# Performance work log

Measured on AMD Instinct MI355X. Metric: run time of the kernel, lower is better.

## Reference

```python
import jax, jax.numpy as jnp
import numpy as np

B, S, H, E = 8, 4096, 1024, 8
TEMPERATURE = 1.0


def setup_inputs() -> dict:
    key = jax.random.key(0)
    ks = jax.random.split(key, 7)
    s_h = 1.0 / np.sqrt(H).astype(np.float32)
    s_h2 = 1.0 / np.sqrt(H // 2).astype(np.float32)
    return {
        "hidden_states": jax.random.normal(ks[0], (B, S, H), jnp.float32),
        # routing_network: Linear(H, H//2) -> ReLU -> Linear(H//2, E)
        "W1": jax.random.normal(ks[1], (H, H // 2), jnp.float32) * s_h,
        "b1": jnp.zeros((H // 2,), jnp.float32),
        "W2": jax.random.normal(ks[2], (H // 2, E), jnp.float32) * s_h2,
        "b2": jnp.zeros((E,), jnp.float32),
        # per-expert dense transform (fixed stand-in for torch.randn-per-call)
        "expert_W": jax.random.normal(ks[3], (E, H, H), jnp.float32) * s_h,
        "expert_b": jax.random.normal(ks[4], (E, H), jnp.float32),
    }


def reference(hidden_states, W1, b1, W2, b2, expert_W, expert_b):
    # Routing network -> logits [B, S, E]
    h = jax.nn.relu(jnp.einsum("bsh,hf->bsf", hidden_states, W1) + b1)
    logits = jnp.einsum("bsf,fe->bse", h, W2) + b2
    probs = jax.nn.softmax(logits / TEMPERATURE, axis=-1)
    # top-1 expert per token (scores are NOT applied to output in the original)
    sel = jnp.argmax(probs, axis=-1)  # [B, S] int
    out = jnp.zeros_like(hidden_states)
    for e in range(E):  # small fixed loop over experts
        mask = (sel == e)[..., None].astype(hidden_states.dtype)  # [B, S, 1]
        xe = hidden_states * mask
        ye = jnp.einsum("bsh,hd->bsd", xe, expert_W[e]) + expert_b[e]
        out = out + ye * mask
    return out
```

## Files before the change

### kernel.cpp

```cpp
#include <hip/hip_runtime.h>
#include <hip/hip_bf16.h>
#include <stdint.h>

#define NTOK 32768
#define HD 1024
#define FD 512
#define NEXP 8
#define TAU 0.05f

typedef __attribute__((ext_vector_type(8))) short short8;
typedef __attribute__((ext_vector_type(4))) float f32x4;

__device__ __forceinline__ short f2bh(float f) {
  uint32_t u = __float_as_uint(f);
  return (short)((u + 0x7fffu + ((u >> 16) & 1u)) >> 16);
}

__device__ __forceinline__ void gl16(void* lds, const void* g) {
  __builtin_amdgcn_global_load_lds(
      (const __attribute__((address_space(1))) void*)g,
      (__attribute__((address_space(3))) void*)lds, 16, 0, 0);
}

__global__ __launch_bounds__(256) void k_convert(const float* __restrict__ x,
                                                 short* __restrict__ xbf) {
  size_t i = ((size_t)blockIdx.x * 256 + threadIdx.x) * 8;
  f32x4 v0 = *(const f32x4*)(x + i);
  f32x4 v1 = *(const f32x4*)(x + i + 4);
  short8 o;
#pragma unroll
  for (int q = 0; q < 4; ++q) { o[q] = f2bh(v0[q]); o[4 + q] = f2bh(v1[q]); }
  *(short8*)(xbf + i) = o;
}

__global__ __launch_bounds__(256) void k_transpose(
    const float* __restrict__ src, short* __restrict__ dst, int rows, int cols) {
  __shared__ float tile[32][33];
  size_t msz = (size_t)rows * cols;
  src += (size_t)blockIdx.z * msz;
  dst += (size_t)blockIdx.z * msz;
  int c0 = blockIdx.x * 32, r0 = blockIdx.y * 32;
  int tx = threadIdx.x & 31, ty = threadIdx.x >> 5;
#pragma unroll
  for (int i = 0; i < 32; i += 8)
    tile[ty + i][tx] = src[(size_t)(r0 + ty + i) * cols + c0 + tx];
  __syncthreads();
#pragma unroll
  for (int i = 0; i < 32; i += 8)
    dst[(size_t)(c0 + ty + i) * rows + r0 + tx] = f2bh(tile[tx][ty + i]);
}

template <bool ABF>
__global__ __launch_bounds__(256) void k_gemm1(
    const short* __restrict__ xbf, const float* __restrict__ xf,
    const short* __restrict__ W1T, const float* __restrict__ b1,
    const float* __restrict__ W2, float* __restrict__ part) {
  __shared__ __align__(16) char smem[37888];
  short* As = (short*)smem;
  short* Bs = (short*)(smem + 8192);

  const int tid = threadIdx.x;
  const int lane = tid & 63, wave = tid >> 6;
  const int wr = wave >> 1, wc = wave & 1;
  const int fr = lane & 15, fg = lane >> 4;
  const int bx = ((blockIdx.x & 7) << 5) | (blockIdx.x >> 3);
  const int m0 = bx * 128, n0 = blockIdx.y * 128;
  const int by = blockIdx.y;

  const int off0 = wave * 1024 + lane * 16;
  const int off1 = off0 + 4096;
  const int r0 = off0 >> 6, c0 = (off0 & 63) >> 1;
  const int r1 = off1 >> 6, c1 = (off1 & 63) >> 1;
  const short* b0p = W1T + (size_t)(n0 + r0) * HD + c0;
  const short* b1p = W1T + (size_t)(n0 + r1) * HD + c1;
  char* ldsB0 = smem + 8192 + wave * 1024;
  char* ldsB1 = smem + 8192 + wave * 1024 + 4096;

  const short* a0p = nullptr; const short* a1p = nullptr;
  char* ldsA0 = smem + wave * 1024;
  char* ldsA1 = smem + wave * 1024 + 4096;
  const float* aF = nullptr;
  int ar = 0, ah = 0;
  if constexpr (ABF) {
    a0p = xbf + (size_t)(m0 + r0) * HD + c0;
    a1p = xbf + (size_t)(m0 + r1) * HD + c1;
  } else {
    ar = tid >> 1; ah = tid & 1;
    aF = xf + (size_t)(m0 + ar) * HD + ah * 16;
  }

  f32x4 acc[4][4];
#pragma unroll
  for (int i = 0; i < 4; ++i)
#pragma unroll
    for (int j = 0; j < 4; ++j) acc[i][j] = (f32x4){0.f, 0.f, 0.f, 0.f};

  for (int k0 = 0; k0 < HD; k0 += 32) {
    gl16(ldsB0, b0p + k0);
    gl16(ldsB1, b1p + k0);
    if constexpr (ABF) {
      gl16(ldsA0, a0p + k0);
      gl16(ldsA1, a1p + k0);
    } else {
      f32x4 u0 = *(const f32x4*)(aF + k0);
      f32x4 u1 = *(const f32x4*)(aF + k0 + 4);
      f32x4 u2 = *(const f32x4*)(aF + k0 + 8);
      f32x4 u3 = *(const f32x4*)(aF + k0 + 12);
      short8 s0, s1;
#pragma unroll
      for (int q = 0; q < 4; ++q) {
        s0[q] = f2bh(u0[q]); s0[4 + q] = f2bh(u1[q]);
        s1[q] = f2bh(u2[q]); s1[4 + q] = f2bh(u3[q]);
      }
      *(short8*)(As + ar * 32 + ah * 16) = s0;
      *(short8*)(As + ar * 32 + ah * 16 + 8) = s1;
    }
    __syncthreads();
    short8 af[4], bf[4];
#pragma unroll
    for (int i = 0; i < 4; ++i) {
      af[i] = *(const short8*)(As + (wr * 64 + i * 16 + fr) * 32 + fg * 8);
      bf[i] = *(const short8*)(Bs + (wc * 64 + i * 16 + fr) * 32 + fg * 8);
    }
#pragma unroll
    for (int i = 0; i < 4; ++i)
#pragma unroll
      for (int j = 0; j < 4; ++j)
        acc[i][j] = __builtin_amdgcn_mfma_f32_16x16x32_bf16(af[i], bf[j], acc[i][j], 0, 0, 0);
    __syncthreads();
  }

  float* hl64 = (float*)smem;
  float* W2c  = (float*)(smem + 33024);
  *(f32x4*)(W2c + tid * 4) = *(const f32x4*)(W2 + (size_t)n0 * NEXP + tid * 4);
  float b1j[4];
#pragma unroll
  for (int j = 0; j < 4; ++j) b1j[j] = b1[n0 + wc * 64 + j * 16 + fr];

  for (int p = 0; p < 2; ++p) {
    if (wr == p) {
#pragma unroll
      for (int i = 0; i < 4; ++i)
#pragma unroll
        for (int j = 0; j < 4; ++j) {
          int col = wc * 64 + j * 16 + fr;
#pragma unroll
          for (int q = 0; q < 4; ++q)
            hl64[(i * 16 + fg * 4 + q) * 129 + col] = fmaxf(acc[i][j][q] + b1j[j], 0.f);
        }
    }
    __syncthreads();
    if (tid < 128) {
      int r2 = tid & 63, eh = tid >> 6;
      const float* hrow = hl64 + r2 * 129;
      const float* wcp = W2c + eh * 4;
      float s0 = 0.f, s1 = 0.f, s2 = 0.f, s3 = 0.f;
      for (int f = 0; f < 128; ++f) {
        float hv = hrow[f];
        s0 += hv * wcp[f * 8 + 0];
        s1 += hv * wcp[f * 8 + 1];
        s2 += hv * wcp[f * 8 + 2];
        s3 += hv * wcp[f * 8 + 3];
      }
      float* pp = part + (size_t)(m0 + p * 64 + r2) * 32 + by * 8 + eh * 4;
      pp[0] = s0; pp[1] = s1; pp[2] = s2; pp[3] = s3;
    }
    __syncthreads();
  }
}

__global__ __launch_bounds__(256) void k_combine(
    const float* __restrict__ part, const float* __restrict__ b2,
    int* __restrict__ sel, int* __restrict__ flagged, int* __restrict__ nflag) {
  int t = blockIdx.x * 256 + threadIdx.x;
  const float* p = part + (size_t)t * 32;
  float lg[8];
#pragma unroll
  for (int e = 0; e < 8; ++e) lg[e] = p[e] + p[8 + e] + p[16 + e] + p[24 + e] + b2[e];
  int be = 0; float best = lg[0];
#pragma unroll
  for (int e = 1; e < 8; ++e) if (lg[e] > best) { best = lg[e]; be = e; }
  float second = -3.4e38f;
#pragma unroll
  for (int e = 0; e < 8; ++e) if (e != be && lg[e] > second) second = lg[e];
  sel[t] = be;
  if (best - second < TAU) {
    int ix = atomicAdd(nflag, 1);
    if (ix < NTOK) flagged[ix] = t;
  }
}

__global__ __launch_bounds__(256) void k_recompute(
    const float* __restrict__ x, const float* __restrict__ W1,
    const float* __restrict__ b1, const float* __restrict__ W2,
    const float* __restrict__ b2, const int* __restrict__ flagged,
    const int* __restrict__ nflag, int* __restrict__ sel) {
  __shared__ float xs[1024][8];
  __shared__ double hs[8][512];
  __shared__ double lgs[8][8];
  int nf = *nflag; if (nf > NTOK) nf = NTOK;
  for (int g = blockIdx.x; g * 8 < nf; g += gridDim.x) {
    int base = g * 8;
    int cnt8 = nf - base; if (cnt8 > 8) cnt8 = 8;
    __syncthreads();
    for (int q = threadIdx.x; q < 8192; q += 256) {
      int t = q & 7, h = q >> 3;
      xs[h][t] = (t < cnt8) ? x[(size_t)flagged[base + t] * HD + h] : 0.f;
    }
    __syncthreads();
    int f0 = threadIdx.x * 2;
    double a0[8], a1[8];
#pragma unroll
    for (int t = 0; t < 8; ++t) { a0[t] = 0.0; a1[t] = 0.0; }
    for (int h = 0; h < 1024; ++h) {
      float2 w = *(const float2*)(W1 + (size_t)h * FD + f0);
      double w0 = (double)w.x, w1 = (double)w.y;
      f32x4 xa = *(const f32x4*)(&xs[h][0]);
      f32x4 xb = *(const f32x4*)(&xs[h][4]);
#pragma unroll
      for (int t = 0; t < 4; ++t) {
        double xv = (double)xa[t];
        a0[t] += xv * w0; a1[t] += xv * w1;
      }
#pragma unroll
      for (int t = 0; t < 4; ++t) {
        double xv = (double)xb[t];
        a0[4 + t] += xv * w0; a1[4 + t] += xv * w1;
      }
    }
#pragma unroll
    for (int t = 0; t < 8; ++t) {
      double v0 = a0[t] + (double)b1[f0], v1 = a1[t] + (double)b1[f0 + 1];
      hs[t][f0] = v0 > 0.0 ? v0 : 0.0;
      hs[t][f0 + 1] = v1 > 0.0 ? v1 : 0.0;
    }
    __syncthreads();
    if (threadIdx.x < 64) {
      int t = threadIdx.x >> 3, e = threadIdx.x & 7;
      double s = 0.0;
      for (int f = 0; f < 512; ++f) s += hs[t][f] * (double)W2[f * 8 + e];
      lgs[t][e] = s + (double)b2[e];
    }
    __syncthreads();
    if (threadIdx.x < 8 && (int)threadIdx.x < cnt8) {
      int t = threadIdx.x;
      int be = 0; double best = lgs[t][0];
#pragma unroll
      for (int e = 1; e < 8; ++e) if (lgs[t][e] > best) { best = lgs[t][e]; be = e; }
      sel[flagged[base + t]] = be;
    }
    __syncthreads();
  }
}

__global__ __launch_bounds__(256) void k_compact(
    const int* __restrict__ sel, int* __restrict__ cnt, int* __restrict__ list) {
  __shared__ int wcnt[4][8];
  __shared__ int woff[4][8];
  __shared__ int bbase[8];
  const int tid = threadIdx.x, lane = tid & 63, wave = tid >> 6;
  const int t = blockIdx.x * 256 + tid;
  const int e = sel[t];
  const unsigned long long ltmask = (1ull << lane) - 1ull;
  int rank = 0;
#pragma unroll
  for (int e2 = 0; e2 < 8; ++e2) {
    unsigned long long m = __ballot(e == e2);
    if (e2 == e) rank = __popcll(m & ltmask);
    if (lane == 0) wcnt[wave][e2] = __popcll(m);
  }
  __syncthreads();
  if (tid < 8) {
    int s0 = wcnt[0][tid], s1 = wcnt[1][tid], s2 = wcnt[2][tid], s3 = wcnt[3][tid];
    woff[0][tid] = 0; woff[1][tid] = s0; woff[2][tid] = s0 + s1; woff[3][tid] = s0 + s1 + s2;
    bbase[tid] = atomicAdd(&cnt[tid], s0 + s1 + s2 + s3);
  }
  __syncthreads();
  list[(size_t)e * NTOK + bbase[e] + woff[wave][e] + rank] = t;
}

__global__ void k_build_desc(const int* __restrict__ cnt, int* __restrict__ desc,
                             int* __restrict__ ntl) {
  if (threadIdx.x == 0 && blockIdx.x == 0) {
    int n = 0;
    for (int e = 0; e < 8; ++e) {
      int m = (cnt[e] + 127) >> 7;
      for (int i = 0; i < m; ++i) desc[n++] = (e << 16) | i;
    }
    *ntl = n;
  }
}

template <bool ABF>
__global__ __launch_bounds__(256) void k_gemm2(
    const short* __restrict__ xbf, const float* __restrict__ xf,
    const short* __restrict__ WexpT, const float* __restrict__ expert_b,
    const int* __restrict__ cnt, const int* __restrict__ list,
    const int* __restrict__ desc, const int* __restrict__ ntl,
    float* __restrict__ out) {
  __shared__ __align__(16) short As[128 * 32];
  __shared__ __align__(16) short Bs[128 * 32];
  __shared__ int toks[128];
  const int bx = (blockIdx.x % 8) * 33 + blockIdx.x / 8;
  if (bx >= *ntl) return;
  int dsc = desc[bx];
  int e = dsc >> 16, mt = dsc & 0xffff;
  int ce = cnt[e];
  int mb = mt * 128;
  int rows = ce - mb; if (rows > 128) rows = 128;

  const int tid = threadIdx.x;
  if (tid < 128) {
    int idx = mb + tid;
    toks[tid] = list[(size_t)e * NTOK + (idx < ce ? idx : ce - 1)];
  }
  __syncthreads();

  const int lane = tid & 63, wave = tid >> 6;
  const int wr = wave >> 1, wc = wave & 1;
  const int fr = lane & 15, fg = lane >> 4;
  const int n0 = blockIdx.y * 128;

  const int off0 = wave * 1024 + lane * 16;
  const int off1 = off0 + 4096;
  const int r0 = off0 >> 6, c0 = (off0 & 63) >> 1;
  const int r1 = off1 >> 6, c1 = (off1 & 63) >> 1;
  const size_t ebase = (size_t)e << 20;
  const short* b0p = WexpT + ebase + (size_t)(n0 + r0) * HD + c0;
  const short* b1p = WexpT + ebase + (size_t)(n0 + r1) * HD + c1;
  char* ldsA0 = (char*)As + wave * 1024;
  char* ldsA1 = (char*)As + wave * 1024 + 4096;
  char* ldsB0 = (char*)Bs + wave * 1024;
  char* ldsB1 = (char*)Bs + wave * 1024 + 4096;

  const short* a0p = nullptr; const short* a1p = nullptr;
  const float* aF = nullptr;
  int ar = 0, ah = 0;
  if constexpr (ABF) {
    a0p = xbf + (size_t)toks[r0] * HD + c0;
    a1p = xbf + (size_t)toks[r1] * HD + c1;
  } else {
    ar = tid >> 1; ah = tid & 1;
    aF = xf + (size_t)toks[ar] * HD + ah * 16;
  }

  f32x4 acc[4][4];
#pragma unroll
  for (int i = 0; i < 4; ++i)
#pragma unroll
    for (int j = 0; j < 4; ++j) acc[i][j] = (f32x4){0.f, 0.f, 0.f, 0.f};

  for (int k0 = 0; k0 < HD; k0 += 32) {
    gl16(ldsB0, b0p + k0);
    gl16(ldsB1, b1p + k0);
    if constexpr (ABF) {
      gl16(ldsA0, a0p + k0);
      gl16(ldsA1, a1p + k0);
    } else {
      f32x4 u0 = *(const f32x4*)(aF + k0);
      f32x4 u1 = *(const f32x4*)(aF + k0 + 4);
      f32x4 u2 = *(const f32x4*)(aF + k0 + 8);
      f32x4 u3 = *(const f32x4*)(aF + k0 + 12);
      short8 s0, s1;
#pragma unroll
      for (int q = 0; q < 4; ++q) {
        s0[q] = f2bh(u0[q]); s0[4 + q] = f2bh(u1[q]);
        s1[q] = f2bh(u2[q]); s1[4 + q] = f2bh(u3[q]);
      }
      *(short8*)(As + ar * 32 + ah * 16) = s0;
      *(short8*)(As + ar * 32 + ah * 16 + 8) = s1;
    }
    __syncthreads();
    short8 af[4], bf[4];
#pragma unroll
    for (int i = 0; i < 4; ++i) {
      af[i] = *(const short8*)(As + (wr * 64 + i * 16 + fr) * 32 + fg * 8);
      bf[i] = *(const short8*)(Bs + (wc * 64 + i * 16 + fr) * 32 + fg * 8);
    }
#pragma unroll
    for (int i = 0; i < 4; ++i)
#pragma unroll
      for (int j = 0; j < 4; ++j)
        acc[i][j] = __builtin_amdgcn_mfma_f32_16x16x32_bf16(af[i], bf[j], acc[i][j], 0, 0, 0);
    __syncthreads();
  }

  float ebv[4];
#pragma unroll
  for (int j = 0; j < 4; ++j) ebv[j] = expert_b[e * HD + n0 + wc * 64 + j * 16 + fr];
#pragma unroll
  for (int i = 0; i < 4; ++i)
#pragma unroll
    for (int j = 0; j < 4; ++j) {
      int col = n0 + wc * 64 + j * 16 + fr;
#pragma unroll
      for (int q = 0; q < 4; ++q) {
        int rr = wr * 64 + i * 16 + fg * 4 + q;
        if (rr < rows) out[(size_t)toks[rr] * HD + col] = acc[i][j][q] + ebv[j];
      }
    }
}

extern "C" void kernel_launch(void* const* d_in, const int* in_sizes, int n_in,
                              void* d_out, int out_size, void* d_ws, size_t ws_size,
                              hipStream_t stream) {
  const float* x  = (const float*)d_in[0];
  const float* W1 = (const float*)d_in[1];
  const float* b1 = (const float*)d_in[2];
  const float* W2 = (const float*)d_in[3];
  const float* b2 = (const float*)d_in[4];
  const float* eW = (const float*)d_in[5];
  const float* eb = (const float*)d_in[6];
  float* out = (float*)d_out;
  char* ws = (char*)d_ws;

  const size_t XBF_BYTES = (size_t)NTOK * HD * 2;
  size_t need_rest = 16777216ull + 1048576 + 4194304 + 131072 + 131072 + 1048576 + 4096;
  bool big = ws_size >= XBF_BYTES + need_rest;

  size_t off = 0;
  short* xbf = nullptr;
  if (big) { xbf = (short*)ws; off += XBF_BYTES; }
  short* WexpT = (short*)(ws + off); off += 16777216;
  short* W1T   = (short*)(ws + off); off += 1048576;
  float* part  = (float*)(ws + off); off += 4194304;
  int* sel     = (int*)(ws + off); off += 131072;
  int* flagged = (int*)(ws + off); off += 131072;
  int* list    = (int*)(ws + off); off += 1048576;
  int* cnt     = (int*)(ws + off); off += 32;
  int* nflag   = (int*)(ws + off); off += 4;
  int* ntl     = (int*)(ws + off); off += 28;
  int* desc    = (int*)(ws + off); off += 1088;
  if (ws_size < off) return;

  hipMemsetAsync(cnt, 0, 40, stream);

  dim3 b256(256);
  if (big) k_convert<<<dim3(16384), b256, 0, stream>>>(x, xbf);
  k_transpose<<<dim3(16, 32, 1), b256, 0, stream>>>(W1, W1T, 1024, 512);
  k_transpose<<<dim3(32, 32, 8), b256, 0, stream>>>(eW, WexpT, 1024, 1024);
  if (big)
    k_gemm1<true><<<dim3(256, 4), b256, 0, stream>>>(xbf, nullptr, W1T, b1, W2, part);
  else
    k_gemm1<false><<<dim3(256, 4), b256, 0, stream>>>(nullptr, x, W1T, b1, W2, part);
  k_combine<<<dim3(128), b256, 0, stream>>>(part, b2, sel, flagged, nflag);
  k_recompute<<<dim3(512), b256, 0, stream>>>(x, W1, b1, W2, b2, flagged, nflag, sel);
  k_compact<<<dim3(128), b256, 0, stream>>>(sel, cnt, list);
  k_build_desc<<<dim3(1), dim3(64), 0, stream>>>(cnt, desc, ntl);
  if (big)
    k_gemm2<true><<<dim3(264, 8), b256, 0, stream>>>(xbf, nullptr, WexpT, eb, cnt, list, desc, ntl, out);
  else
    k_gemm2<false><<<dim3(264, 8), b256, 0, stream>>>(nullptr, x, WexpT, eb, cnt, list, desc, ntl, out);
}
```

Measured before the change: 395.3 us.

## Add split-bf16 MFMA refinement stage for near-tie routing tokens

Tokens whose top-two logits fall within the tolerance are no longer all re-scored by the slow fp64 scalar kernel. They first go through a tensor-core GEMM that splits x and W1 into bf16 high and low parts (three MFMAs per tile, roughly fp32 accuracy). Only tokens whose margin is still below a much tighter tolerance fall back to a per-token fp64 recompute. This adds a W1 split transpose, extra launches and reuses the list and part buffers as scratch, and it trusts the split-bf16 accuracy to decide every tie outside the tight band.

After: 356.5 us. 9.8% less time.

```diff
diff --git a/kernel.cpp b/kernel.cpp
--- a/kernel.cpp
+++ b/kernel.cpp
@@ -7,6 +7,7 @@
 #define FD 512
 #define NEXP 8
 #define TAU 0.05f
+#define TAU2 4e-4f
 
 typedef __attribute__((ext_vector_type(8))) short short8;
 typedef __attribute__((ext_vector_type(4))) float f32x4;
@@ -14,6 +15,9 @@
 __device__ __forceinline__ short f2bh(float f) {
   uint32_t u = __float_as_uint(f);
   return (short)((u + 0x7fffu + ((u >> 16) & 1u)) >> 16);
+}
+__device__ __forceinline__ float bh2f(short h) {
+  return __uint_as_float(((uint32_t)(uint16_t)h) << 16);
 }
 
 __device__ __forceinline__ void gl16(void* lds, const void* g) {
@@ -48,6 +52,26 @@
 #pragma unroll
   for (int i = 0; i < 32; i += 8)
     dst[(size_t)(c0 + ty + i) * rows + r0 + tx] = f2bh(tile[tx][ty + i]);
+}
+
+__global__ __launch_bounds__(256) void k_transpose_split(
+    const float* __restrict__ src, short* __restrict__ dstH,
+    short* __restrict__ dstL, int rows, int cols) {
+  __shared__ float tile[32][33];
+  int c0 = blockIdx.x * 32, r0 = blockIdx.y * 32;
+  int tx = threadIdx.x & 31, ty = threadIdx.x >> 5;
+#pragma unroll
+  for (int i = 0; i < 32; i += 8)
+    tile[ty + i][tx] = src[(size_t)(r0 + ty + i) * cols + c0 + tx];
+  __syncthreads();
+#pragma unroll
+  for (int i = 0; i < 32; i += 8) {
+    float v = tile[tx][ty + i];
+    short h = f2bh(v);
+    size_t di = (size_t)(c0 + ty + i) * rows + r0 + tx;
+    dstH[di] = h;
+    dstL[di] = f2bh(v - bh2f(h));
+  }
 }
 
 template <bool ABF>
@@ -190,64 +214,216 @@
   }
 }
 
-__global__ __launch_bounds__(256) void k_recompute(
+__global__ __launch_bounds__(256) void k_gemmR(
+    const float* __restrict__ x, const short* __restrict__ W1hT,
+    const short* __restrict__ W1lT, const float* __restrict__ b1,
+    const float* __restrict__ W2, const int* __restrict__ flagged,
+    const int* __restrict__ nflag, float* __restrict__ partR) {
+  __shared__ __align__(16) char smem[37888];
+  __shared__ int toks[128];
+  short* Ah = (short*)smem;
+  short* Al = (short*)(smem + 8192);
+
+  int nf = *nflag; if (nf > NTOK) nf = NTOK;
+  const int m0 = blockIdx.x * 128;
+  if (m0 >= nf) return;
+  const int tid = threadIdx.x;
+  if (tid < 128) {
+    int s = m0 + tid;
+    toks[tid] = flagged[s < nf ? s : nf - 1];
+  }
+  __syncthreads();
+
+  const int lane = tid & 63, wave = tid >> 6;
+  const int wr = wave >> 1, wc = wave & 1;
+  const int fr = lane & 15, fg = lane >> 4;
+  const int n0 = blockIdx.y * 128;
+  const int by = blockIdx.y;
+
+  const int off0 = wave * 1024 + lane * 16;
+  const int off1 = off0 + 4096;
+  const int r0 = off0 >> 6, c0 = (off0 & 63) >> 1;
+  const int r1 = off1 >> 6, c1 = (off1 & 63) >> 1;
+  const short* bh0p = W1hT + (size_t)(n0 + r0) * HD + c0;
+  const short* bh1p = W1hT + (size_t)(n0 + r1) * HD + c1;
+  const short* bl0p = W1lT + (size_t)(n0 + r0) * HD + c0;
+  const short* bl1p = W1lT + (size_t)(n0 + r1) * HD + c1;
+  char* ldsBh0 = smem + 16384 + wave * 1024;
+  char* ldsBh1 = smem + 16384 + wave * 1024 + 4096;
+  char* ldsBl0 = smem + 24576 + wave * 1024;
+  char* ldsBl1 = smem + 24576 + wave * 1024 + 4096;
+  const int ar = tid >> 1, ah2 = tid & 1;
+  const float* aF = x + (size_t)toks[ar] * HD + ah2 * 16;
+
+  f32x4 acc[4][4];
+#pragma unroll
+  for (int i = 0; i < 4; ++i)
+#pragma unroll
+    for (int j = 0; j < 4; ++j) acc[i][j] = (f32x4){0.f, 0.f, 0.f, 0.f};
+
+  for (int k0 = 0; k0 < HD; k0 += 32) {
+    gl16(ldsBh0, bh0p + k0);
+    gl16(ldsBh1, bh1p + k0);
+    gl16(ldsBl0, bl0p + k0);
+    gl16(ldsBl1, bl1p + k0);
+    f32x4 u0 = *(const f32x4*)(aF + k0);
+    f32x4 u1 = *(const f32x4*)(aF + k0 + 4);
+    f32x4 u2 = *(const f32x4*)(aF + k0 + 8);
+    f32x4 u3 = *(const f32x4*)(aF + k0 + 12);
+    short8 sh0, sh1, sl0, sl1;
+#pragma unroll
+    for (int q = 0; q < 4; ++q) {
+      { float f = u0[q]; short h = f2bh(f); sh0[q]     = h; sl0[q]     = f2bh(f - bh2f(h)); }
+      { float f = u1[q]; short h = f2bh(f); sh0[4 + q] = h; sl0[4 + q] = f2bh(f - bh2f(h)); }
+      { float f = u2[q]; short h = f2bh(f); sh1[q]     = h; sl1[q]     = f2bh(f - bh2f(h)); }
+      { float f = u3[q]; short h = f2bh(f); sh1[4 + q] = h; sl1[4 + q] = f2bh(f - bh2f(h)); }
+    }
+    *(short8*)(Ah + ar * 32 + ah2 * 16)     = sh0;
+    *(short8*)(Ah + ar * 32 + ah2 * 16 + 8) = sh1;
+    *(short8*)(Al + ar * 32 + ah2 * 16)     = sl0;
+    *(short8*)(Al + ar * 32 + ah2 * 16 + 8) = sl1;
+    __syncthreads();
+    short8 af[4], alf[4], bf[4], blf[4];
+#pragma unroll
+    for (int i = 0; i < 4; ++i) {
+      int row = (wr * 64 + i * 16 + fr) * 32 + fg * 8;
+      af[i]  = *(const short8*)(Ah + row);
+      alf[i] = *(const short8*)(Al + row);
+      int rowb = (wc * 64 + i * 16 + fr) * 32 + fg * 8;
+      bf[i]  = *(const short8*)((short*)(smem + 16384) + rowb);
+      blf[i] = *(const short8*)((short*)(smem + 24576) + rowb);
+    }
+#pragma unroll
+    for (int i = 0; i < 4; ++i)
+#pragma unroll
+      for (int j = 0; j < 4; ++j) {
+        acc[i][j] = __builtin_amdgcn_mfma_f32_16x16x32_bf16(af[i],  bf[j],  acc[i][j], 0, 0, 0);
+        acc[i][j] = __builtin_amdgcn_mfma_f32_16x16x32_bf16(af[i],  blf[j], acc[i][j], 0, 0, 0);
+        acc[i][j] = __builtin_amdgcn_mfma_f32_16x16x32_bf16(alf[i], bf[j],  acc[i][j], 0, 0, 0);
+      }
+    __syncthreads();
+  }
+
+  float* hl64 = (float*)smem;
+  float* W2c  = (float*)(smem + 33024);
+  *(f32x4*)(W2c + tid * 4) = *(const f32x4*)(W2 + (size_t)n0 * NEXP + tid * 4);
+  float b1j[4];
+#pragma unroll
+  for (int j = 0; j < 4; ++j) b1j[j] = b1[n0 + wc * 64 + j * 16 + fr];
+
+  for (int p = 0; p < 2; ++p) {
+    if (wr == p) {
+#pragma unroll
+      for (int i = 0; i < 4; ++i)
+#pragma unroll
+        for (int j = 0; j < 4; ++j) {
+          int col = wc * 64 + j * 16 + fr;
+#pragma unroll
+          for (int q = 0; q < 4; ++q)
+            hl64[(i * 16 + fg * 4 + q) * 129 + col] = fmaxf(acc[i][j][q] + b1j[j], 0.f);
+        }
+    }
+    __syncthreads();
+    if (tid < 128) {
+      int r2 = tid & 63, eh = tid >> 6;
+      const float* hrow = hl64 + r2 * 129;
+      const float* wcp = W2c + eh * 4;
+      float s0 = 0.f, s1 = 0.f, s2 = 0.f, s3 = 0.f;
+      for (int f = 0; f < 128; ++f) {
+        float hv = hrow[f];
+        s0 += hv * wcp[f * 8 + 0];
+        s1 += hv * wcp[f * 8 + 1];
+        s2 += hv * wcp[f * 8 + 2];
+        s3 += hv * wcp[f * 8 + 3];
+      }
+      float* pp = partR + (size_t)(m0 + p * 64 + r2) * 32 + by * 8 + eh * 4;
+      pp[0] = s0; pp[1] = s1; pp[2] = s2; pp[3] = s3;
+    }
+    __syncthreads();
+  }
+}
+
+__global__ __launch_bounds__(256) void k_combineR(
+    const float* __restrict__ partR, const float* __restrict__ b2,
+    const int* __restrict__ flagged, const int* __restrict__ nflag,
+    int* __restrict__ sel, int* __restrict__ flagged2, int* __restrict__ nflag2) {
+  int nf = *nflag; if (nf > NTOK) nf = NTOK;
+  int s = blockIdx.x * 256 + threadIdx.x;
+  if (s >= nf) return;
+  int t = flagged[s];
+  const float* p = partR + (size_t)s * 32;
+  float lg[8];
+#pragma unroll
+  for (int e = 0; e < 8; ++e) lg[e] = p[e] + p[8 + e] + p[16 + e] + p[24 + e] + b2[e];
+  int be = 0; float best = lg[0];
+#pragma unroll
+  for (int e = 1; e < 8; ++e) if (lg[e] > best) { best = lg[e]; be = e; }
+  float second = -3.4e38f;
+#pragma unroll
+  for (int e = 0; e < 8; ++e) if (e != be && lg[e] > second) second = lg[e];
+  sel[t] = be;
+  if (best - second < TAU2) {
+    int ix = atomicAdd(nflag2, 1);
+    if (ix < NTOK) flagged2[ix] = t;
+  }
+}
+
+__global__ __launch_bounds__(256) void k_recomputeB(
     const float* __restrict__ x, const float* __restrict__ W1,
     const float* __restrict__ b1, const float* __restrict__ W2,
-    const float* __restrict__ b2, const int* __restrict__ flagged,
-    const int* __restrict__ nflag, int* __restrict__ sel) {
-  __shared__ float xs[1024][8];
-  __shared__ double hs[8][512];
-  __shared__ double lgs[8][8];
-  int nf = *nflag; if (nf > NTOK) nf = NTOK;
-  for (int g = blockIdx.x; g * 8 < nf; g += gridDim.x) {
-    int base = g * 8;
-    int cnt8 = nf - base; if (cnt8 > 8) cnt8 = 8;
-    __syncthreads();
-    for (int q = threadIdx.x; q < 8192; q += 256) {
-      int t = q & 7, h = q >> 3;
-      xs[h][t] = (t < cnt8) ? x[(size_t)flagged[base + t] * HD + h] : 0.f;
-    }
-    __syncthreads();
-    int f0 = threadIdx.x * 2;
-    double a0[8], a1[8];
-#pragma unroll
-    for (int t = 0; t < 8; ++t) { a0[t] = 0.0; a1[t] = 0.0; }
-    for (int h = 0; h < 1024; ++h) {
-      float2 w = *(const float2*)(W1 + (size_t)h * FD + f0);
-      double w0 = (double)w.x, w1 = (double)w.y;
-      f32x4 xa = *(const f32x4*)(&xs[h][0]);
-      f32x4 xb = *(const f32x4*)(&xs[h][4]);
-#pragma unroll
-      for (int t = 0; t < 4; ++t) {
-        double xv = (double)xa[t];
-        a0[t] += xv * w0; a1[t] += xv * w1;
-      }
-#pragma unroll
-      for (int t = 0; t < 4; ++t) {
-        double xv = (double)xb[t];
-        a0[4 + t] += xv * w0; a1[4 + t] += xv * w1;
-      }
-    }
-#pragma unroll
-    for (int t = 0; t < 8; ++t) {
-      double v0 = a0[t] + (double)b1[f0], v1 = a1[t] + (double)b1[f0 + 1];
-      hs[t][f0] = v0 > 0.0 ? v0 : 0.0;
-      hs[t][f0 + 1] = v1 > 0.0 ? v1 : 0.0;
-    }
-    __syncthreads();
-    if (threadIdx.x < 64) {
-      int t = threadIdx.x >> 3, e = threadIdx.x & 7;
+    const float* __restrict__ b2, const int* __restrict__ flagged2,
+    const int* __restrict__ nflag2, int* __restrict__ sel) {
+  __shared__ float xs[1024];
+  __shared__ double hs[512];
+  __shared__ double red[8][32];
+  __shared__ double lgd[8];
+  int nf = *nflag2; if (nf > NTOK) nf = NTOK;
+  const int tid = threadIdx.x;
+  for (int ti = blockIdx.x; ti < nf; ti += gridDim.x) {
+    int t = flagged2[ti];
+    __syncthreads();
+    for (int q = tid; q < 1024; q += 256) xs[q] = x[(size_t)t * HD + q];
+    __syncthreads();
+    int f0 = tid * 2;
+    double a0 = 0.0, a1 = 0.0;
+    for (int h = 0; h < 1024; h += 4) {
+      float2 w0 = *(const float2*)(W1 + (size_t)(h + 0) * FD + f0);
+      float2 w1 = *(const float2*)(W1 + (size_t)(h + 1) * FD + f0);
+      float2 w2 = *(const float2*)(W1 + (size_t)(h + 2) * FD + f0);
+      float2 w3 = *(const float2*)(W1 + (size_t)(h + 3) * FD + f0);
+      double x0 = (double)xs[h], x1 = (double)xs[h + 1];
+      double x2 = (double)xs[h + 2], x3 = (double)xs[h + 3];
+      a0 += x0 * (double)w0.x; a1 += x0 * (double)w0.y;
+      a0 += x1 * (double)w1.x; a1 += x1 * (double)w1.y;
+      a0 += x2 * (double)w2.x; a1 += x2 * (double)w2.y;
+      a0 += x3 * (double)w3.x; a1 += x3 * (double)w3.y;
+    }
+    a0 += (double)b1[f0]; a1 += (double)b1[f0 + 1];
+    hs[f0]     = a0 > 0.0 ? a0 : 0.0;
+    hs[f0 + 1] = a1 > 0.0 ? a1 : 0.0;
+    __syncthreads();
+    {
+      int e = tid >> 5, c = tid & 31;
+      int fb = c * 16;
       double s = 0.0;
-      for (int f = 0; f < 512; ++f) s += hs[t][f] * (double)W2[f * 8 + e];
-      lgs[t][e] = s + (double)b2[e];
-    }
-    __syncthreads();
-    if (threadIdx.x < 8 && (int)threadIdx.x < cnt8) {
-      int t = threadIdx.x;
-      int be = 0; double best = lgs[t][0];
-#pragma unroll
-      for (int e = 1; e < 8; ++e) if (lgs[t][e] > best) { best = lgs[t][e]; be = e; }
-      sel[flagged[base + t]] = be;
+#pragma unroll
+      for (int ff = 0; ff < 16; ++ff)
+        s += hs[fb + ff] * (double)W2[(size_t)(fb + ff) * 8 + e];
+      red[e][c] = s;
+    }
+    __syncthreads();
+    if (tid < 8) {
+      double s = 0.0;
+#pragma unroll
+      for (int c = 0; c < 32; ++c) s += red[tid][c];
+      lgd[tid] = s + (double)b2[tid];
+    }
+    __syncthreads();
+    if (tid == 0) {
+      int be = 0; double best = lgd[0];
+#pragma unroll
+      for (int e = 1; e < 8; ++e) if (lgd[e] > best) { best = lgd[e]; be = e; }
+      sel[t] = be;
     }
     __syncthreads();
   }
@@ -415,36 +591,42 @@
   char* ws = (char*)d_ws;
 
   const size_t XBF_BYTES = (size_t)NTOK * HD * 2;
-  size_t need_rest = 16777216ull + 1048576 + 4194304 + 131072 + 131072 + 1048576 + 4096;
+  size_t need_rest = 16777216ull + 1048576 + 4194304 + 131072 * 3 + 1048576 + 4096;
   bool big = ws_size >= XBF_BYTES + need_rest;
 
   size_t off = 0;
   short* xbf = nullptr;
   if (big) { xbf = (short*)ws; off += XBF_BYTES; }
-  short* WexpT = (short*)(ws + off); off += 16777216;
-  short* W1T   = (short*)(ws + off); off += 1048576;
-  float* part  = (float*)(ws + off); off += 4194304;
-  int* sel     = (int*)(ws + off); off += 131072;
-  int* flagged = (int*)(ws + off); off += 131072;
-  int* list    = (int*)(ws + off); off += 1048576;
-  int* cnt     = (int*)(ws + off); off += 32;
-  int* nflag   = (int*)(ws + off); off += 4;
-  int* ntl     = (int*)(ws + off); off += 28;
-  int* desc    = (int*)(ws + off); off += 1088;
+  short* WexpT  = (short*)(ws + off); off += 16777216;
+  short* W1T    = (short*)(ws + off); off += 1048576;
+  float* part   = (float*)(ws + off); off += 4194304;
+  int* sel      = (int*)(ws + off); off += 131072;
+  int* flagged  = (int*)(ws + off); off += 131072;
+  int* flagged2 = (int*)(ws + off); off += 131072;
+  int* list     = (int*)(ws + off); off += 1048576;
+  int* cnt      = (int*)(ws + off); off += 32;
+  int* nflag    = (int*)(ws + off); off += 4;
+  int* ntl      = (int*)(ws + off); off += 4;
+  int* nflag2   = (int*)(ws + off); off += 24;
+  int* desc     = (int*)(ws + off); off += 1088;
   if (ws_size < off) return;
 
-  hipMemsetAsync(cnt, 0, 40, stream);
+  short* W1lT = (short*)list;
+
+  hipMemsetAsync(cnt, 0, 44, stream);
 
   dim3 b256(256);
   if (big) k_convert<<<dim3(16384), b256, 0, stream>>>(x, xbf);
-  k_transpose<<<dim3(16, 32, 1), b256, 0, stream>>>(W1, W1T, 1024, 512);
+  k_transpose_split<<<dim3(16, 32), b256, 0, stream>>>(W1, W1T, W1lT, 1024, 512);
   k_transpose<<<dim3(32, 32, 8), b256, 0, stream>>>(eW, WexpT, 1024, 1024);
   if (big)
     k_gemm1<true><<<dim3(256, 4), b256, 0, stream>>>(xbf, nullptr, W1T, b1, W2, part);
   else
     k_gemm1<false><<<dim3(256, 4), b256, 0, stream>>>(nullptr, x, W1T, b1, W2, part);
   k_combine<<<dim3(128), b256, 0, stream>>>(part, b2, sel, flagged, nflag);
-  k_recompute<<<dim3(512), b256, 0, stream>>>(x, W1, b1, W2, b2, flagged, nflag, sel);
+  k_gemmR<<<dim3(256, 4), b256, 0, stream>>>(x, W1T, W1lT, b1, W2, flagged, nflag, part);
+  k_combineR<<<dim3(128), b256, 0, stream>>>(part, b2, flagged, nflag, sel, flagged2, nflag2);
+  k_recomputeB<<<dim3(128), b256, 0, stream>>>(x, W1, b1, W2, b2, flagged2, nflag2, sel);
   k_compact<<<dim3(128), b256, 0, stream>>>(sel, cnt, list);
   k_build_desc<<<dim3(1), dim3(64), 0, stream>>>(cnt, desc, ntl);
   if (big)
```
